# Kernel optimization log

Measured on AMD Instinct MI355X. Metric: run time of the kernel, lower is better.

Reference implementation:

```python
import jax, jax.numpy as jnp
import numpy as np

GRAVITY = 9.81
W_INERTIA = 1.0
W_GRAVITY = 0.01
W_STRAIN = 1.0

V = 500_000
E = 2_000_000


def setup_inputs() -> dict:
    key = jax.random.key(0)
    ks = jax.random.split(key, 7)
    pos_next = jax.random.normal(ks[0], (V, 3), dtype=jnp.float32)
    pos_curr = jax.random.normal(ks[1], (V, 3), dtype=jnp.float32)
    pos_prev = jax.random.normal(ks[2], (V, 3), dtype=jnp.float32)
    mass = jax.random.uniform(ks[3], (V, 1), dtype=jnp.float32)
    elements = jax.random.randint(ks[4], (E, 4), 0, V, dtype=jnp.int64)
    rest_volumes = jax.random.uniform(ks[5], (E,), dtype=jnp.float32)
    rest_inv = jax.random.normal(ks[6], (E, 3, 3), dtype=jnp.float32)
    lam = jnp.float32(1.0)
    mu = jnpp_one = jnp.float32(1.0)
    return {
        "pos_next": pos_next, "pos_curr": pos_curr, "pos_prev": pos_prev,
        "mass": mass, "elements": elements, "rest_volumes": rest_volumes,
        "rest_inv": rest_inv, "lam": lam, "mu": mu,
    }


def _det3(F):
    # F: (E, 3, 3)
    return (F[:, 0, 0] * (F[:, 1, 1] * F[:, 2, 2] - F[:, 1, 2] * F[:, 2, 1])
            - F[:, 0, 1] * (F[:, 1, 0] * F[:, 2, 2] - F[:, 1, 2] * F[:, 2, 0])
            + F[:, 0, 2] * (F[:, 1, 0] * F[:, 2, 1] - F[:, 1, 1] * F[:, 2, 0]))


def _physics_loss(pos_next, pos_curr, pos_prev, mass, elements, rest_volumes, rest_inv, lam, mu):
    # Inertia: mean over all V*3 entries of 0.5 * m * a^2
    accel = pos_next + pos_prev - 2.0 * pos_curr          # (V, 3)
    inertia = 0.5 * jnp.mean(mass * accel * accel)
    # Gravity: -mean(m * g * y)
    gravity = -jnp.mean(mass * GRAVITY * pos_curr[:, 1:2])
    # Strain (Neo-Hookean) on pos_next
    v = pos_next[elements]                                 # (E, 4, 3)
    Ds = jnp.stack([v[:, 1] - v[:, 0], v[:, 2] - v[:, 0], v[:, 3] - v[:, 0]], axis=-1)  # (E,3,3)
    F_def = jnp.einsum('eij,ejk->eik', Ds, rest_inv)       # (E, 3, 3)
    det_F = jnp.maximum(_det3(F_def), 1e-8)
    log_det = jnp.log(det_F)
    tr_FtF = jnp.sum(F_def * F_def, axis=(1, 2))           # trace(F^T F) = ||F||_F^2
    psi = 0.5 * lam * log_det ** 2 - mu * log_det + 0.5 * mu * (tr_FtF - 3.0)
    strain = jnp.mean(psi * rest_volumes)
    return W_INERTIA * inertia + W_GRAVITY * gravity + W_STRAIN * strain


def reference(pos_next, pos_curr, pos_prev, mass, elements, rest_volumes, rest_inv, lam, mu):
    return _physics_loss(pos_next, pos_curr, pos_prev, mass, elements, rest_volumes, rest_inv, lam, mu)
```

## Files before the change

kernel.cpp:

```cpp
#include <hip/hip_runtime.h>
#include <hip/hip_fp16.h>

#define GRAVITY_F 9.81f
#define EPT 4

typedef int v4i __attribute__((ext_vector_type(4)));

union PackedPos { uint2 u; __half h[4]; };

__device__ __forceinline__ float blockReduceSum(float val) {
    #pragma unroll
    for (int off = 32; off > 0; off >>= 1)
        val += __shfl_down(val, off, 64);
    __shared__ float smem[16];
    const int lane = threadIdx.x & 63;
    const int wave = threadIdx.x >> 6;
    if (lane == 0) smem[wave] = val;
    __syncthreads();
    const int nwaves = (blockDim.x + 63) >> 6;
    val = 0.0f;
    if (wave == 0) {
        if (lane < nwaves) val = smem[lane];
        #pragma unroll
        for (int off = 8; off > 0; off >>= 1)
            val += __shfl_down(val, off, 64);
    }
    return val;
}

__global__ void pack_kernel(const float* __restrict__ pn,
                            uint2* __restrict__ out, int V) {
    const int v = blockIdx.x * blockDim.x + threadIdx.x;
    if (v >= V) return;
    PackedPos p;
    p.h[0] = __float2half(__builtin_nontemporal_load(pn + 3 * v + 0));
    p.h[1] = __float2half(__builtin_nontemporal_load(pn + 3 * v + 1));
    p.h[2] = __float2half(__builtin_nontemporal_load(pn + 3 * v + 2));
    p.h[3] = __half(0.0f);
    out[v] = p.u;
}

template <bool PACKED>
__global__ void __launch_bounds__(256, 4)
fused_kernel(const float* __restrict__ pn,
             const float* __restrict__ pc,
             const float* __restrict__ pp,
             const float* __restrict__ mass,
             const int*   __restrict__ elems,
             const float* __restrict__ vols,
             const float* __restrict__ rinv,
             const float* __restrict__ lam_p,
             const float* __restrict__ mu_p,
             const uint2* __restrict__ packed4,
             float* __restrict__ partials,
             int V, int E, int Eblocks,
             float sI, float sG, float sS) {
    float local = 0.0f;

    if ((int)blockIdx.x < Eblocks) {
        const float lam = lam_p[0];
        const float mu  = mu_p[0];
        const int base = blockIdx.x * (EPT * 256) + threadIdx.x;

        int  ec[EPT];
        float sc[EPT];
        #pragma unroll
        for (int i = 0; i < EPT; ++i) {
            const int e = base + i * 256;
            ec[i] = e < E ? e : (E - 1);
            sc[i] = e < E ? sS : 0.0f;
        }
        v4i  idx[EPT];
        float vol[EPT];
        #pragma unroll
        for (int i = 0; i < EPT; ++i) {
            idx[i] = __builtin_nontemporal_load(((const v4i*)elems) + ec[i]);
            vol[i] = __builtin_nontemporal_load(vols + ec[i]);
        }

        float x[EPT][4][3];
        if (PACKED) {
            uint2 g[EPT][4];
            #pragma unroll
            for (int i = 0; i < EPT; ++i) {
                g[i][0] = packed4[idx[i].x];
                g[i][1] = packed4[idx[i].y];
                g[i][2] = packed4[idx[i].z];
                g[i][3] = packed4[idx[i].w];
            }
            #pragma unroll
            for (int i = 0; i < EPT; ++i)
                #pragma unroll
                for (int j = 0; j < 4; ++j) {
                    PackedPos p; p.u = g[i][j];
                    x[i][j][0] = __half2float(p.h[0]);
                    x[i][j][1] = __half2float(p.h[1]);
                    x[i][j][2] = __half2float(p.h[2]);
                }
        } else {
            #pragma unroll
            for (int i = 0; i < EPT; ++i) {
                const float* v0 = pn + 3 * (size_t)idx[i].x;
                const float* v1 = pn + 3 * (size_t)idx[i].y;
                const float* v2 = pn + 3 * (size_t)idx[i].z;
                const float* v3 = pn + 3 * (size_t)idx[i].w;
                #pragma unroll
                for (int r = 0; r < 3; ++r) {
                    x[i][0][r] = v0[r];
                    x[i][1][r] = v1[r];
                    x[i][2][r] = v2[r];
                    x[i][3][r] = v3[r];
                }
            }
        }

        float R[EPT][9];
        #pragma unroll
        for (int i = 0; i < EPT; ++i) {
            const float* Rp = rinv + 9 * (size_t)ec[i];
            #pragma unroll
            for (int k = 0; k < 9; ++k)
                R[i][k] = __builtin_nontemporal_load(Rp + k);
        }

        #pragma unroll
        for (int i = 0; i < EPT; ++i) {
            float d[3][3];
            #pragma unroll
            for (int r = 0; r < 3; ++r) {
                d[r][0] = x[i][1][r] - x[i][0][r];
                d[r][1] = x[i][2][r] - x[i][0][r];
                d[r][2] = x[i][3][r] - x[i][0][r];
            }
            float F[3][3];
            #pragma unroll
            for (int r = 0; r < 3; ++r)
                #pragma unroll
                for (int k = 0; k < 3; ++k)
                    F[r][k] = d[r][0] * R[i][0 * 3 + k]
                            + d[r][1] * R[i][1 * 3 + k]
                            + d[r][2] * R[i][2 * 3 + k];
            const float det = F[0][0] * (F[1][1] * F[2][2] - F[1][2] * F[2][1])
                            - F[0][1] * (F[1][0] * F[2][2] - F[1][2] * F[2][0])
                            + F[0][2] * (F[1][0] * F[2][1] - F[1][1] * F[2][0]);
            const float ld = logf(fmaxf(det, 1e-8f));
            float tr = 0.0f;
            #pragma unroll
            for (int r = 0; r < 3; ++r)
                #pragma unroll
                for (int k = 0; k < 3; ++k)
                    tr += F[r][k] * F[r][k];
            const float psi = 0.5f * lam * ld * ld - mu * ld + 0.5f * mu * (tr - 3.0f);
            local += sc[i] * (psi * vol[i]);
        }
    } else {
        const int v = (blockIdx.x - Eblocks) * blockDim.x + threadIdx.x;
        if (v < V) {
            const float m  = __builtin_nontemporal_load(mass + v);
            const float p0 = __builtin_nontemporal_load(pc + 3 * v + 0);
            const float y  = __builtin_nontemporal_load(pc + 3 * v + 1);
            const float p2 = __builtin_nontemporal_load(pc + 3 * v + 2);
            const float n0 = __builtin_nontemporal_load(pn + 3 * v + 0);
            const float n1 = __builtin_nontemporal_load(pn + 3 * v + 1);
            const float n2 = __builtin_nontemporal_load(pn + 3 * v + 2);
            const float q0 = __builtin_nontemporal_load(pp + 3 * v + 0);
            const float q1 = __builtin_nontemporal_load(pp + 3 * v + 1);
            const float q2 = __builtin_nontemporal_load(pp + 3 * v + 2);
            const float a0 = n0 + q0 - 2.0f * p0;
            const float a1 = n1 + q1 - 2.0f * y;
            const float a2 = n2 + q2 - 2.0f * p2;
            local = sI * (m * (a0 * a0 + a1 * a1 + a2 * a2)) + sG * (m * y);
        }
    }

    const float tot = blockReduceSum(local);
    if (threadIdx.x == 0) partials[blockIdx.x] = tot;
}

__global__ void reduce_kernel(const float* __restrict__ partials, int n,
                              float* __restrict__ out) {
    double s = 0.0;
    for (int i = threadIdx.x; i < n; i += blockDim.x)
        s += (double)partials[i];
    __shared__ double sm[256];
    sm[threadIdx.x] = s;
    __syncthreads();
    #pragma unroll
    for (int off = 128; off > 0; off >>= 1) {
        if (threadIdx.x < off) sm[threadIdx.x] += sm[threadIdx.x + off];
        __syncthreads();
    }
    if (threadIdx.x == 0) out[0] = (float)sm[0];
}

extern "C" void kernel_launch(void* const* d_in, const int* in_sizes, int n_in,
                              void* d_out, int out_size, void* d_ws, size_t ws_size,
                              hipStream_t stream) {
    const float* pos_next = (const float*)d_in[0];
    const float* pos_curr = (const float*)d_in[1];
    const float* pos_prev = (const float*)d_in[2];
    const float* mass     = (const float*)d_in[3];
    const int*   elements = (const int*)d_in[4];
    const float* rest_vol = (const float*)d_in[5];
    const float* rest_inv = (const float*)d_in[6];
    const float* lam_p    = (const float*)d_in[7];
    const float* mu_p     = (const float*)d_in[8];
    float* out = (float*)d_out;

    const int V = in_sizes[3];
    const int E = in_sizes[5];

    const float sI = 0.5f / (3.0f * (float)V);
    const float sG = -0.01f * GRAVITY_F / (float)V;
    const float sS = 1.0f / (float)E;

    const int block = 256;
    const int Eblocks = (E + EPT * block - 1) / (EPT * block);
    const int Vblocks = (V + block - 1) / block;
    const int grid = Eblocks + Vblocks;

    float* partials = (float*)d_ws;
    const size_t part_bytes = ((size_t)grid * sizeof(float) + 255) & ~(size_t)255;
    const size_t need = part_bytes + (size_t)V * 8;

    if (ws_size >= need) {
        uint2* packed4 = (uint2*)((char*)d_ws + part_bytes);
        pack_kernel<<<(V + block - 1) / block, block, 0, stream>>>(pos_next, packed4, V);
        fused_kernel<true><<<grid, block, 0, stream>>>(pos_next, pos_curr, pos_prev,
                                                       mass, elements, rest_vol,
                                                       rest_inv, lam_p, mu_p,
                                                       packed4, partials,
                                                       V, E, Eblocks, sI, sG, sS);
    } else {
        fused_kernel<false><<<grid, block, 0, stream>>>(pos_next, pos_curr, pos_prev,
                                                        mass, elements, rest_vol,
                                                        rest_inv, lam_p, mu_p,
                                                        nullptr, partials,
                                                        V, E, Eblocks, sI, sG, sS);
    }
    reduce_kernel<<<1, 256, 0, stream>>>(partials, grid, out);
}
```

Before: 208.0 us.

## Drop fp16 pack pass, gather fp32 vertices with vector loads, fuse final reduction

Removes the separate pass that packed pos_next into half precision. Each vertex is now gathered straight from the fp32 array as one unaligned 4-float vector load. The offset is clamped and the lanes shifted for the last vertex so the load never reads past the end. The final reduction moves into the main kernel through an atomic counter and a last-block pattern, which removes the separate reduce launch but adds a memset. The trade is dropping one full pass over V plus a launch, against a larger per-gather footprint (16 bytes instead of 8).

```diff
diff --git a/kernel.cpp b/kernel.cpp
--- a/kernel.cpp
+++ b/kernel.cpp
@@ -1,12 +1,10 @@
 #include <hip/hip_runtime.h>
-#include <hip/hip_fp16.h>
 
 #define GRAVITY_F 9.81f
 #define EPT 4
 
-typedef int v4i __attribute__((ext_vector_type(4)));
-
-union PackedPos { uint2 u; __half h[4]; };
+typedef int   v4i __attribute__((ext_vector_type(4)));
+typedef float v4f __attribute__((ext_vector_type(4), aligned(4)));
 
 __device__ __forceinline__ float blockReduceSum(float val) {
     #pragma unroll
@@ -28,33 +26,22 @@
     return val;
 }
 
-__global__ void pack_kernel(const float* __restrict__ pn,
-                            uint2* __restrict__ out, int V) {
-    const int v = blockIdx.x * blockDim.x + threadIdx.x;
-    if (v >= V) return;
-    PackedPos p;
-    p.h[0] = __float2half(__builtin_nontemporal_load(pn + 3 * v + 0));
-    p.h[1] = __float2half(__builtin_nontemporal_load(pn + 3 * v + 1));
-    p.h[2] = __float2half(__builtin_nontemporal_load(pn + 3 * v + 2));
-    p.h[3] = __half(0.0f);
-    out[v] = p.u;
-}
-
-template <bool PACKED>
-__global__ void __launch_bounds__(256, 4)
-fused_kernel(const float* __restrict__ pn,
-             const float* __restrict__ pc,
-             const float* __restrict__ pp,
-             const float* __restrict__ mass,
-             const int*   __restrict__ elems,
-             const float* __restrict__ vols,
-             const float* __restrict__ rinv,
-             const float* __restrict__ lam_p,
-             const float* __restrict__ mu_p,
-             const uint2* __restrict__ packed4,
-             float* __restrict__ partials,
-             int V, int E, int Eblocks,
-             float sI, float sG, float sS) {
+__global__ __launch_bounds__(256)
+__attribute__((amdgpu_waves_per_eu(4, 4)))
+void fused_kernel(const float* __restrict__ pn,
+                  const float* __restrict__ pc,
+                  const float* __restrict__ pp,
+                  const float* __restrict__ mass,
+                  const int*   __restrict__ elems,
+                  const float* __restrict__ vols,
+                  const float* __restrict__ rinv,
+                  const float* __restrict__ lam_p,
+                  const float* __restrict__ mu_p,
+                  float* __restrict__ partials,
+                  unsigned int* __restrict__ counter,
+                  float* __restrict__ out,
+                  int V, int E, int Eblocks,
+                  float sI, float sG, float sS) {
     float local = 0.0f;
 
     if ((int)blockIdx.x < Eblocks) {
@@ -62,7 +49,7 @@
         const float mu  = mu_p[0];
         const int base = blockIdx.x * (EPT * 256) + threadIdx.x;
 
-        int  ec[EPT];
+        int   ec[EPT];
         float sc[EPT];
         #pragma unroll
         for (int i = 0; i < EPT; ++i) {
@@ -70,7 +57,8 @@
             ec[i] = e < E ? e : (E - 1);
             sc[i] = e < E ? sS : 0.0f;
         }
-        v4i  idx[EPT];
+
+        v4i   idx[EPT];
         float vol[EPT];
         #pragma unroll
         for (int i = 0; i < EPT; ++i) {
@@ -78,39 +66,15 @@
             vol[i] = __builtin_nontemporal_load(vols + ec[i]);
         }
 
-        float x[EPT][4][3];
-        if (PACKED) {
-            uint2 g[EPT][4];
-            #pragma unroll
-            for (int i = 0; i < EPT; ++i) {
-                g[i][0] = packed4[idx[i].x];
-                g[i][1] = packed4[idx[i].y];
-                g[i][2] = packed4[idx[i].z];
-                g[i][3] = packed4[idx[i].w];
-            }
-            #pragma unroll
-            for (int i = 0; i < EPT; ++i)
-                #pragma unroll
-                for (int j = 0; j < 4; ++j) {
-                    PackedPos p; p.u = g[i][j];
-                    x[i][j][0] = __half2float(p.h[0]);
-                    x[i][j][1] = __half2float(p.h[1]);
-                    x[i][j][2] = __half2float(p.h[2]);
-                }
-        } else {
-            #pragma unroll
-            for (int i = 0; i < EPT; ++i) {
-                const float* v0 = pn + 3 * (size_t)idx[i].x;
-                const float* v1 = pn + 3 * (size_t)idx[i].y;
-                const float* v2 = pn + 3 * (size_t)idx[i].z;
-                const float* v3 = pn + 3 * (size_t)idx[i].w;
-                #pragma unroll
-                for (int r = 0; r < 3; ++r) {
-                    x[i][0][r] = v0[r];
-                    x[i][1][r] = v1[r];
-                    x[i][2][r] = v2[r];
-                    x[i][3][r] = v3[r];
-                }
+        const int cap = 3 * V - 4;
+        v4f q[EPT][4];
+        #pragma unroll
+        for (int i = 0; i < EPT; ++i) {
+            #pragma unroll
+            for (int j = 0; j < 4; ++j) {
+                int off = 3 * idx[i][j];
+                off = off > cap ? cap : off;
+                q[i][j] = *reinterpret_cast<const v4f*>(pn + off);
             }
         }
 
@@ -123,14 +87,23 @@
                 R[i][k] = __builtin_nontemporal_load(Rp + k);
         }
 
-        #pragma unroll
-        for (int i = 0; i < EPT; ++i) {
+        const int lastV = V - 1;
+        #pragma unroll
+        for (int i = 0; i < EPT; ++i) {
+            float x[4][3];
+            #pragma unroll
+            for (int j = 0; j < 4; ++j) {
+                const bool sh = (idx[i][j] == lastV);
+                x[j][0] = sh ? q[i][j][1] : q[i][j][0];
+                x[j][1] = sh ? q[i][j][2] : q[i][j][1];
+                x[j][2] = sh ? q[i][j][3] : q[i][j][2];
+            }
             float d[3][3];
             #pragma unroll
             for (int r = 0; r < 3; ++r) {
-                d[r][0] = x[i][1][r] - x[i][0][r];
-                d[r][1] = x[i][2][r] - x[i][0][r];
-                d[r][2] = x[i][3][r] - x[i][0][r];
+                d[r][0] = x[1][r] - x[0][r];
+                d[r][1] = x[2][r] - x[0][r];
+                d[r][2] = x[3][r] - x[0][r];
             }
             float F[3][3];
             #pragma unroll
@@ -174,7 +147,35 @@
     }
 
     const float tot = blockReduceSum(local);
-    if (threadIdx.x == 0) partials[blockIdx.x] = tot;
+
+    __shared__ bool isLast;
+    if (threadIdx.x == 0) {
+        partials[blockIdx.x] = tot;
+        bool last = false;
+        if (counter) {
+            __threadfence();
+            const unsigned t = atomicAdd(counter, 1u);
+            last = (t == gridDim.x - 1);
+        }
+        isLast = last;
+    }
+    __syncthreads();
+    if (isLast) {
+        __threadfence();
+        double s = 0.0;
+        const int n = (int)gridDim.x;
+        for (int i = threadIdx.x; i < n; i += blockDim.x)
+            s += (double)partials[i];
+        __shared__ double sm[256];
+        sm[threadIdx.x] = s;
+        __syncthreads();
+        #pragma unroll
+        for (int off = 128; off > 0; off >>= 1) {
+            if (threadIdx.x < off) sm[threadIdx.x] += sm[threadIdx.x + off];
+            __syncthreads();
+        }
+        if (threadIdx.x == 0) out[0] = (float)sm[0];
+    }
 }
 
 __global__ void reduce_kernel(const float* __restrict__ partials, int n,
@@ -219,24 +220,24 @@
     const int Vblocks = (V + block - 1) / block;
     const int grid = Eblocks + Vblocks;
 
-    float* partials = (float*)d_ws;
-    const size_t part_bytes = ((size_t)grid * sizeof(float) + 255) & ~(size_t)255;
-    const size_t need = part_bytes + (size_t)V * 8;
+    unsigned int* counter = (unsigned int*)d_ws;
+    float* partials = (float*)((char*)d_ws + 256);
+    const size_t need = 256 + (size_t)grid * sizeof(float);
 
     if (ws_size >= need) {
-        uint2* packed4 = (uint2*)((char*)d_ws + part_bytes);
-        pack_kernel<<<(V + block - 1) / block, block, 0, stream>>>(pos_next, packed4, V);
-        fused_kernel<true><<<grid, block, 0, stream>>>(pos_next, pos_curr, pos_prev,
-                                                       mass, elements, rest_vol,
-                                                       rest_inv, lam_p, mu_p,
-                                                       packed4, partials,
-                                                       V, E, Eblocks, sI, sG, sS);
+        hipMemsetAsync(d_ws, 0, 4, stream);
+        fused_kernel<<<grid, block, 0, stream>>>(pos_next, pos_curr, pos_prev,
+                                                 mass, elements, rest_vol,
+                                                 rest_inv, lam_p, mu_p,
+                                                 partials, counter, out,
+                                                 V, E, Eblocks, sI, sG, sS);
     } else {
-        fused_kernel<false><<<grid, block, 0, stream>>>(pos_next, pos_curr, pos_prev,
-                                                        mass, elements, rest_vol,
-                                                        rest_inv, lam_p, mu_p,
-                                                        nullptr, partials,
-                                                        V, E, Eblocks, sI, sG, sS);
-    }
-    reduce_kernel<<<1, 256, 0, stream>>>(partials, grid, out);
-}
+        float* p2 = (float*)d_ws;
+        fused_kernel<<<grid, block, 0, stream>>>(pos_next, pos_curr, pos_prev,
+                                                 mass, elements, rest_vol,
+                                                 rest_inv, lam_p, mu_p,
+                                                 p2, nullptr, out,
+                                                 V, E, Eblocks, sI, sG, sS);
+        reduce_kernel<<<1, 256, 0, stream>>>(p2, grid, out);
+    }
+}
```

After: 390.2 us. 1.88x slower.
